# Performance work log

Measured on AMD Instinct MI355X. Metric: run time of the kernel, lower is better.

## Reference

```python
import jax, jax.numpy as jnp
import numpy as np

H = 64  # hidden size

def _lstm_layer(x_btf, w_ih, w_hh, b_ih, b_hh):
    """One LSTM layer, batch_first input x_btf [B,T,F]. PyTorch gate order i,f,g,o."""
    B = x_btf.shape[0]
    # Precompute input contribution for all timesteps: [T,B,4H]
    xg = jnp.einsum('btf,gf->tbg', x_btf, w_ih) + (b_ih + b_hh)
    h0 = jnp.zeros((B, H), dtype=x_btf.dtype)
    c0 = jnp.zeros((B, H), dtype=x_btf.dtype)

    def step(carry, xg_t):
        h, c = carry
        gates = xg_t + h @ w_hh.T  # [B,4H]
        i, f, g, o = jnp.split(gates, 4, axis=-1)
        i = jax.nn.sigmoid(i)
        f = jax.nn.sigmoid(f)
        g = jnp.tanh(g)
        o = jax.nn.sigmoid(o)
        c_new = f * c + i * g
        h_new = o * jnp.tanh(c_new)
        return (h_new, c_new), h_new

    (h_T, c_T), hs = jax.lax.scan(step, (h0, c0), xg)
    return jnp.transpose(hs, (1, 0, 2)), h_T, c_T  # [B,T,H], [B,H], [B,H]


def setup_inputs() -> dict:
    key = jax.random.key(0)
    ks = jax.random.split(key, 9)
    s_in = 1.0 / np.sqrt(H)
    inp = {
        'x': jax.random.normal(ks[0], (512, 2048, 4), dtype=jnp.float32),
        'w_ih_l0': jax.random.uniform(ks[1], (4 * H, 4), jnp.float32, -s_in, s_in),
        'w_hh_l0': jax.random.uniform(ks[2], (4 * H, H), jnp.float32, -s_in, s_in),
        'b_ih_l0': jax.random.uniform(ks[3], (4 * H,), jnp.float32, -s_in, s_in),
        'b_hh_l0': jax.random.uniform(ks[4], (4 * H,), jnp.float32, -s_in, s_in),
        'w_ih_l1': jax.random.uniform(ks[5], (4 * H, H), jnp.float32, -s_in, s_in),
        'w_hh_l1': jax.random.uniform(ks[6], (4 * H, H), jnp.float32, -s_in, s_in),
        'b_ih_l1': jax.random.uniform(ks[7], (4 * H,), jnp.float32, -s_in, s_in),
        'b_hh_l1': jax.random.uniform(ks[8], (4 * H,), jnp.float32, -s_in, s_in),
    }
    return inp


def reference(x, w_ih_l0, w_hh_l0, b_ih_l0, b_hh_l0, w_ih_l1, w_hh_l1, b_ih_l1, b_hh_l1):
    out0, h0, c0 = _lstm_layer(x, w_ih_l0, w_hh_l0, b_ih_l0, b_hh_l0)
    out1, h1, c1 = _lstm_layer(out0, w_ih_l1, w_hh_l1, b_ih_l1, b_hh_l1)
    h_n = jnp.stack([h0, h1], axis=0)  # [num_layers, B, H]
    c_n = jnp.stack([c0, c1], axis=0)
    return out1, (h_n, c_n)
```

## Files before the change

kernel.cpp:

```cpp
#include <hip/hip_runtime.h>

#define T_STEPS 2048
#define HID 64

typedef __attribute__((ext_vector_type(4))) int   int4v;
typedef __attribute__((ext_vector_type(4))) float f32x4;

static __device__ __forceinline__ float exp2_f(float x) {
#if __has_builtin(__builtin_amdgcn_exp2f)
    return __builtin_amdgcn_exp2f(x);
#else
    return exp2f(x);
#endif
}
#define NLOG2E 1.4426950408889634f

__global__ void __launch_bounds__(512, 1) __attribute__((amdgpu_waves_per_eu(2, 2)))
lstm2_i8(const float* __restrict__ x,
         const float* __restrict__ wih0, const float* __restrict__ whh0,
         const float* __restrict__ bih0, const float* __restrict__ bhh0,
         const float* __restrict__ wih1, const float* __restrict__ whh1,
         const float* __restrict__ bih1, const float* __restrict__ bhh1,
         float* __restrict__ out, int B)
{
    __shared__ __align__(16) char s_h0q[2][2][HID];
    __shared__ __align__(16) char s_h1q[2][2][HID];
    __shared__ __align__(16) float s_xf[2 * T_STEPS * 4];

    const int tid  = threadIdx.x;
    const int lane = tid & 63;
    const int wv   = tid >> 6;
    const int wg   = wv >> 2;
    const int wl   = wv & 3;
    const int l15  = lane & 15;
    const int lg   = lane >> 4;
    const int b0   = 2 * blockIdx.x;
    const int u    = 16 * wl + l15;
    const int bx   = lg & 1;
    const int rsel = (l15 >> 2) & 1;

    const float SCL[4] = {-NLOG2E, -NLOG2E, -2.0f * NLOG2E, -NLOG2E};

    const float4* __restrict__ xb4 = (const float4*)(x + (size_t)b0 * (T_STEPS * 4));
    float4* s_xf4 = (float4*)s_xf;
    for (int i2 = tid; i2 < 2 * T_STEPS; i2 += 512) s_xf4[i2] = xb4[i2];
    if (tid < 256) {
        ((char*)s_h0q)[tid] = 0;
        ((char*)s_h1q)[tid] = 0;
    }

    const size_t BTH = (size_t)B * T_STEPS * HID;
    const size_t BH  = (size_t)B * HID;
    const size_t bi  = (size_t)(b0 + bx) * HID + u;
    const int4v Zi = {0, 0, 0, 0};

    auto pack16 = [&](const float* wr, float qs) {
        int4v r;
        #pragma unroll
        for (int dw = 0; dw < 4; ++dw) {
            unsigned d = 0;
            #pragma unroll
            for (int bbb = 0; bbb < 4; ++bbb) {
                int q = (int)rintf(wr[dw * 4 + bbb] * qs);
                d |= ((unsigned)(q & 255)) << (8 * bbb);
            }
            r[dw] = (int)d;
        }
        return r;
    };
    auto rowmax = [&](const float* wr) {
        float mx = 0.f;
        #pragma unroll
        for (int j = 0; j < 16; ++j) mx = fmaxf(mx, fabsf(wr[j]));
        mx = fmaxf(mx, __shfl_xor(mx, 16));
        mx = fmaxf(mx, __shfl_xor(mx, 32));
        return fmaxf(mx, 1e-20f);
    };

    #define BAR() do { asm volatile("s_waitcnt lgkmcnt(0)" ::: "memory"); \
                       __builtin_amdgcn_s_barrier(); } while (0)

    if (wg == 0) {
        int4v W0q[4];
        float dq0[4];
        float wx[4][4];
        float b0s[4];
        #pragma unroll
        for (int ni = 0; ni < 4; ++ni) {
            const int g = 64 * ni + u;
            float wr[16];
            #pragma unroll
            for (int j = 0; j < 16; ++j) wr[j] = whh0[g * HID + 16 * lg + j];
            float mx = rowmax(wr);
            W0q[ni] = pack16(wr, 127.f / mx);
            dq0[ni] = (mx / (127.f * 127.f)) * SCL[ni];
            #pragma unroll
            for (int j = 0; j < 4; ++j) wx[ni][j] = wih0[g * 4 + j] * SCL[ni];
            b0s[ni] = (bih0[g] + bhh0[g]) * SCL[ni];
        }
        float c0s = 0.f, h0s = 0.f;
        const float* xcur = &s_xf[(size_t)bx * T_STEPS * 4];
        __syncthreads();

        auto l0_body = [&](int P) {
            const int Q = P ^ 1;
            const int4v Ha = *(const int4v*)&s_h0q[Q][rsel][16 * lg];
            const float4 xt = *(const float4*)xcur;  xcur += 4;
            __builtin_amdgcn_s_setprio(1);
            int4v a0 = __builtin_amdgcn_mfma_i32_16x16x64_i8(Ha, W0q[0], Zi, 0, 0, 0);
            int4v a1 = __builtin_amdgcn_mfma_i32_16x16x64_i8(Ha, W0q[1], Zi, 0, 0, 0);
            int4v a2 = __builtin_amdgcn_mfma_i32_16x16x64_i8(Ha, W0q[2], Zi, 0, 0, 0);
            int4v a3 = __builtin_amdgcn_mfma_i32_16x16x64_i8(Ha, W0q[3], Zi, 0, 0, 0);
            __builtin_amdgcn_s_setprio(0);
            float t0 = fmaf(wx[0][0], xt.x, b0s[0]);
            float t1 = fmaf(wx[1][0], xt.x, b0s[1]);
            float t2 = fmaf(wx[2][0], xt.x, b0s[2]);
            float t3 = fmaf(wx[3][0], xt.x, b0s[3]);
            t0 = fmaf(wx[0][1], xt.y, t0); t0 = fmaf(wx[0][2], xt.z, t0); t0 = fmaf(wx[0][3], xt.w, t0);
            t1 = fmaf(wx[1][1], xt.y, t1); t1 = fmaf(wx[1][2], xt.z, t1); t1 = fmaf(wx[1][3], xt.w, t1);
            t2 = fmaf(wx[2][1], xt.y, t2); t2 = fmaf(wx[2][2], xt.z, t2); t2 = fmaf(wx[2][3], xt.w, t2);
            t3 = fmaf(wx[3][1], xt.y, t3); t3 = fmaf(wx[3][2], xt.z, t3); t3 = fmaf(wx[3][3], xt.w, t3);
            float s0 = fmaf((float)a0[0], dq0[0], t0);
            float s1 = fmaf((float)a1[0], dq0[1], t1);
            float s2 = fmaf((float)a2[0], dq0[2], t2);
            float s3 = fmaf((float)a3[0], dq0[3], t3);
            float i_ = __builtin_amdgcn_rcpf(1.0f + exp2_f(s0));
            float f_ = __builtin_amdgcn_rcpf(1.0f + exp2_f(s1));
            float g_ = fmaf(2.0f, __builtin_amdgcn_rcpf(1.0f + exp2_f(s2)), -1.0f);
            float o_ = __builtin_amdgcn_rcpf(1.0f + exp2_f(s3));
            c0s = fmaf(f_, c0s, i_ * g_);
            h0s = o_ * fmaf(2.0f, __builtin_amdgcn_rcpf(1.0f + exp2_f(c0s * (-2.0f * NLOG2E))), -1.0f);
            if (lg < 2) s_h0q[P][lg][u] = (char)(int)rintf(h0s * 127.f);
        };

        for (int it = 0; it < T_STEPS / 2; ++it) {
            l0_body(0); BAR();
            l0_body(1); BAR();
        }
        if (lg < 2) {
            out[BTH + bi]          = h0s;
            out[BTH + 2 * BH + bi] = c0s;
        }
    } else {
        int4v Wihq[4], Whhq[4];
        float dqih[4], dqhh[4], b1s[4];
        #pragma unroll
        for (int ni = 0; ni < 4; ++ni) {
            const int g = 64 * ni + u;
            float wr[16];
            #pragma unroll
            for (int j = 0; j < 16; ++j) wr[j] = wih1[g * HID + 16 * lg + j];
            float mxi = rowmax(wr);
            Wihq[ni] = pack16(wr, 127.f / mxi);
            dqih[ni] = (mxi / (127.f * 127.f)) * SCL[ni];
            #pragma unroll
            for (int j = 0; j < 16; ++j) wr[j] = whh1[g * HID + 16 * lg + j];
            float mxh = rowmax(wr);
            Whhq[ni] = pack16(wr, 127.f / mxh);
            dqhh[ni] = (mxh / (127.f * 127.f)) * SCL[ni];
            b1s[ni] = (bih1[g] + bhh1[g]) * SCL[ni];
        }
        float c1s = 0.f, h1s = 0.f;
        float* __restrict__ opp = out + (size_t)(b0 + bx) * T_STEPS * HID + u;
        __syncthreads();
        BAR();

        auto l1_body = [&](int P) {
            const int Q = P ^ 1;
            const int4v Ha = *(const int4v*)&s_h0q[Q][rsel][16 * lg];
            const int4v Ga = *(const int4v*)&s_h1q[Q][rsel][16 * lg];
            __builtin_amdgcn_s_setprio(1);
            int4v dH0 = __builtin_amdgcn_mfma_i32_16x16x64_i8(Ha, Wihq[0], Zi, 0, 0, 0);
            int4v dH1 = __builtin_amdgcn_mfma_i32_16x16x64_i8(Ha, Wihq[1], Zi, 0, 0, 0);
            int4v dH2 = __builtin_amdgcn_mfma_i32_16x16x64_i8(Ha, Wihq[2], Zi, 0, 0, 0);
            int4v dH3 = __builtin_amdgcn_mfma_i32_16x16x64_i8(Ha, Wihq[3], Zi, 0, 0, 0);
            int4v dG0 = __builtin_amdgcn_mfma_i32_16x16x64_i8(Ga, Whhq[0], Zi, 0, 0, 0);
            int4v dG1 = __builtin_amdgcn_mfma_i32_16x16x64_i8(Ga, Whhq[1], Zi, 0, 0, 0);
            int4v dG2 = __builtin_amdgcn_mfma_i32_16x16x64_i8(Ga, Whhq[2], Zi, 0, 0, 0);
            int4v dG3 = __builtin_amdgcn_mfma_i32_16x16x64_i8(Ga, Whhq[3], Zi, 0, 0, 0);
            __builtin_amdgcn_s_setprio(0);
            float s0 = fmaf((float)dG0[0], dqhh[0], fmaf((float)dH0[0], dqih[0], b1s[0]));
            float s1 = fmaf((float)dG1[0], dqhh[1], fmaf((float)dH1[0], dqih[1], b1s[1]));
            float s2 = fmaf((float)dG2[0], dqhh[2], fmaf((float)dH2[0], dqih[2], b1s[2]));
            float s3 = fmaf((float)dG3[0], dqhh[3], fmaf((float)dH3[0], dqih[3], b1s[3]));
            float i_ = __builtin_amdgcn_rcpf(1.0f + exp2_f(s0));
            float f_ = __builtin_amdgcn_rcpf(1.0f + exp2_f(s1));
            float g_ = fmaf(2.0f, __builtin_amdgcn_rcpf(1.0f + exp2_f(s2)), -1.0f);
            float o_ = __builtin_amdgcn_rcpf(1.0f + exp2_f(s3));
            c1s = fmaf(f_, c1s, i_ * g_);
            h1s = o_ * fmaf(2.0f, __builtin_amdgcn_rcpf(1.0f + exp2_f(c1s * (-2.0f * NLOG2E))), -1.0f);
            if (lg < 2) {
                s_h1q[P][lg][u] = (char)(int)rintf(h1s * 127.f);
                *opp = h1s;
            }
            opp += HID;
        };

        for (int it = 0; it < T_STEPS / 2 - 1; ++it) {
            l1_body(1); BAR();
            l1_body(0); BAR();
        }
        l1_body(1); BAR();
        l1_body(0);
        if (lg < 2) {
            out[BTH + BH + bi]     = h1s;
            out[BTH + 3 * BH + bi] = c1s;
        }
    }
    #undef BAR
}

extern "C" void kernel_launch(void* const* d_in, const int* in_sizes, int n_in,
                              void* d_out, int out_size, void* d_ws, size_t ws_size,
                              hipStream_t stream) {
    const float* x    = (const float*)d_in[0];
    const float* wih0 = (const float*)d_in[1];
    const float* whh0 = (const float*)d_in[2];
    const float* bih0 = (const float*)d_in[3];
    const float* bhh0 = (const float*)d_in[4];
    const float* wih1 = (const float*)d_in[5];
    const float* whh1 = (const float*)d_in[6];
    const float* bih1 = (const float*)d_in[7];
    const float* bhh1 = (const float*)d_in[8];
    float* out = (float*)d_out;

    const int B = in_sizes[0] / (T_STEPS * 4);

    lstm2_i8<<<dim3(B / 2), dim3(512), 0, stream>>>(
        x, wih0, whh0, bih0, bhh0, wih1, whh1, bih1, bhh1, out, B);
}
```

Before: 649.5 us.

## Split gate columns across 16 waves with shuffle exchange and MFMA-fused bias

Doubles the block to 1024 threads (8 waves per layer), so each wave computes only two gate tiles per step instead of four. Lanes swap gate pre-activations with a cross-lane shuffle to assemble i,f,g,o. The bias is quantized and folded into the MFMA accumulator input, and layer 1 chains its input and recurrent MFMAs by sharing one row scale across both weight matrices. This shortens the per-wave critical path of each serial timestep, at the cost of barriers over more waves, an extra shuffle, and coarser quantization from the shared scale and integer bias.

```diff
diff --git a/kernel.cpp b/kernel.cpp
--- a/kernel.cpp
+++ b/kernel.cpp
@@ -3,8 +3,7 @@
 #define T_STEPS 2048
 #define HID 64
 
-typedef __attribute__((ext_vector_type(4))) int   int4v;
-typedef __attribute__((ext_vector_type(4))) float f32x4;
+typedef __attribute__((ext_vector_type(4))) int int4v;
 
 static __device__ __forceinline__ float exp2_f(float x) {
 #if __has_builtin(__builtin_amdgcn_exp2f)
@@ -15,13 +14,13 @@
 }
 #define NLOG2E 1.4426950408889634f
 
-__global__ void __launch_bounds__(512, 1) __attribute__((amdgpu_waves_per_eu(2, 2)))
-lstm2_i8(const float* __restrict__ x,
-         const float* __restrict__ wih0, const float* __restrict__ whh0,
-         const float* __restrict__ bih0, const float* __restrict__ bhh0,
-         const float* __restrict__ wih1, const float* __restrict__ whh1,
-         const float* __restrict__ bih1, const float* __restrict__ bhh1,
-         float* __restrict__ out, int B)
+__global__ void __launch_bounds__(1024, 1) __attribute__((amdgpu_waves_per_eu(4, 4)))
+lstm2_w16(const float* __restrict__ x,
+          const float* __restrict__ wih0, const float* __restrict__ whh0,
+          const float* __restrict__ bih0, const float* __restrict__ bhh0,
+          const float* __restrict__ wih1, const float* __restrict__ whh1,
+          const float* __restrict__ bih1, const float* __restrict__ bhh1,
+          float* __restrict__ out, int B)
 {
     __shared__ __align__(16) char s_h0q[2][2][HID];
     __shared__ __align__(16) char s_h1q[2][2][HID];
@@ -30,20 +29,29 @@
     const int tid  = threadIdx.x;
     const int lane = tid & 63;
     const int wv   = tid >> 6;
-    const int wg   = wv >> 2;
-    const int wl   = wv & 3;
+    const int wg   = wv >> 3;
+    const int wl   = wv & 7;
+    const int base = 8 * wl;
     const int l15  = lane & 15;
     const int lg   = lane >> 4;
+    const int l8   = l15 & 7;
+    const int h8   = l15 >> 3;
     const int b0   = 2 * blockIdx.x;
-    const int u    = 16 * wl + l15;
     const int bx   = lg & 1;
     const int rsel = (l15 >> 2) & 1;
+    const int un   = base + l8;
 
     const float SCL[4] = {-NLOG2E, -NLOG2E, -2.0f * NLOG2E, -NLOG2E};
+    const int   tP = h8;
+    const int   tQ = 2 + h8;
+    const int   rP = 64 * tP + un;
+    const int   rQ = 64 * tQ + un;
+    const float aselQ = h8 ? 1.0f : 2.0f;
+    const float cselQ = h8 ? 0.0f : -1.0f;
 
     const float4* __restrict__ xb4 = (const float4*)(x + (size_t)b0 * (T_STEPS * 4));
     float4* s_xf4 = (float4*)s_xf;
-    for (int i2 = tid; i2 < 2 * T_STEPS; i2 += 512) s_xf4[i2] = xb4[i2];
+    for (int i2 = tid; i2 < 2 * T_STEPS; i2 += 1024) s_xf4[i2] = xb4[i2];
     if (tid < 256) {
         ((char*)s_h0q)[tid] = 0;
         ((char*)s_h1q)[tid] = 0;
@@ -51,8 +59,6 @@
 
     const size_t BTH = (size_t)B * T_STEPS * HID;
     const size_t BH  = (size_t)B * HID;
-    const size_t bi  = (size_t)(b0 + bx) * HID + u;
-    const int4v Zi = {0, 0, 0, 0};
 
     auto pack16 = [&](const float* wr, float qs) {
         int4v r;
@@ -60,43 +66,47 @@
         for (int dw = 0; dw < 4; ++dw) {
             unsigned d = 0;
             #pragma unroll
-            for (int bbb = 0; bbb < 4; ++bbb) {
-                int q = (int)rintf(wr[dw * 4 + bbb] * qs);
-                d |= ((unsigned)(q & 255)) << (8 * bbb);
+            for (int bb = 0; bb < 4; ++bb) {
+                int q = (int)rintf(wr[dw * 4 + bb] * qs);
+                d |= ((unsigned)(q & 255)) << (8 * bb);
             }
             r[dw] = (int)d;
         }
         return r;
     };
-    auto rowmax = [&](const float* wr) {
-        float mx = 0.f;
-        #pragma unroll
-        for (int j = 0; j < 16; ++j) mx = fmaxf(mx, fabsf(wr[j]));
-        mx = fmaxf(mx, __shfl_xor(mx, 16));
-        mx = fmaxf(mx, __shfl_xor(mx, 32));
-        return fmaxf(mx, 1e-20f);
-    };
 
     #define BAR() do { asm volatile("s_waitcnt lgkmcnt(0)" ::: "memory"); \
                        __builtin_amdgcn_s_barrier(); } while (0)
 
     if (wg == 0) {
-        int4v W0q[4];
-        float dq0[4];
-        float wx[4][4];
-        float b0s[4];
-        #pragma unroll
-        for (int ni = 0; ni < 4; ++ni) {
-            const int g = 64 * ni + u;
-            float wr[16];
-            #pragma unroll
-            for (int j = 0; j < 16; ++j) wr[j] = whh0[g * HID + 16 * lg + j];
-            float mx = rowmax(wr);
-            W0q[ni] = pack16(wr, 127.f / mx);
-            dq0[ni] = (mx / (127.f * 127.f)) * SCL[ni];
-            #pragma unroll
-            for (int j = 0; j < 4; ++j) wx[ni][j] = wih0[g * 4 + j] * SCL[ni];
-            b0s[ni] = (bih0[g] + bhh0[g]) * SCL[ni];
+        float wrP[16], wrQ[16];
+        #pragma unroll
+        for (int j = 0; j < 16; ++j) {
+            wrP[j] = whh0[rP * HID + 16 * lg + j];
+            wrQ[j] = whh0[rQ * HID + 16 * lg + j];
+        }
+        float mxP = 0.f, mxQ = 0.f;
+        #pragma unroll
+        for (int j = 0; j < 16; ++j) {
+            mxP = fmaxf(mxP, fabsf(wrP[j]));
+            mxQ = fmaxf(mxQ, fabsf(wrQ[j]));
+        }
+        mxP = fmaxf(mxP, __shfl_xor(mxP, 16)); mxP = fmaxf(mxP, __shfl_xor(mxP, 32));
+        mxQ = fmaxf(mxQ, __shfl_xor(mxQ, 16)); mxQ = fmaxf(mxQ, __shfl_xor(mxQ, 32));
+        mxP = fmaxf(mxP, 1e-20f); mxQ = fmaxf(mxQ, 1e-20f);
+        const int4v WPq = pack16(wrP, 127.f / mxP);
+        const int4v WQq = pack16(wrQ, 127.f / mxQ);
+        const float dqP = (mxP / 16129.f) * SCL[tP];
+        const float dqQ = (mxQ / 16129.f) * SCL[tQ];
+        const int bP = (int)rintf((bih0[rP] + bhh0[rP]) * 16129.f / mxP);
+        const int bQ = (int)rintf((bih0[rQ] + bhh0[rQ]) * 16129.f / mxQ);
+        const int4v BiasP = {bP, bP, bP, bP};
+        const int4v BiasQ = {bQ, bQ, bQ, bQ};
+        float wxP[4], wxQ[4];
+        #pragma unroll
+        for (int j = 0; j < 4; ++j) {
+            wxP[j] = wih0[rP * 4 + j] * SCL[tP];
+            wxQ[j] = wih0[rQ * 4 + j] * SCL[tQ];
         }
         float c0s = 0.f, h0s = 0.f;
         const float* xcur = &s_xf[(size_t)bx * T_STEPS * 4];
@@ -107,61 +117,69 @@
             const int4v Ha = *(const int4v*)&s_h0q[Q][rsel][16 * lg];
             const float4 xt = *(const float4*)xcur;  xcur += 4;
             __builtin_amdgcn_s_setprio(1);
-            int4v a0 = __builtin_amdgcn_mfma_i32_16x16x64_i8(Ha, W0q[0], Zi, 0, 0, 0);
-            int4v a1 = __builtin_amdgcn_mfma_i32_16x16x64_i8(Ha, W0q[1], Zi, 0, 0, 0);
-            int4v a2 = __builtin_amdgcn_mfma_i32_16x16x64_i8(Ha, W0q[2], Zi, 0, 0, 0);
-            int4v a3 = __builtin_amdgcn_mfma_i32_16x16x64_i8(Ha, W0q[3], Zi, 0, 0, 0);
+            int4v aP = __builtin_amdgcn_mfma_i32_16x16x64_i8(Ha, WPq, BiasP, 0, 0, 0);
+            int4v aQ = __builtin_amdgcn_mfma_i32_16x16x64_i8(Ha, WQq, BiasQ, 0, 0, 0);
             __builtin_amdgcn_s_setprio(0);
-            float t0 = fmaf(wx[0][0], xt.x, b0s[0]);
-            float t1 = fmaf(wx[1][0], xt.x, b0s[1]);
-            float t2 = fmaf(wx[2][0], xt.x, b0s[2]);
-            float t3 = fmaf(wx[3][0], xt.x, b0s[3]);
-            t0 = fmaf(wx[0][1], xt.y, t0); t0 = fmaf(wx[0][2], xt.z, t0); t0 = fmaf(wx[0][3], xt.w, t0);
-            t1 = fmaf(wx[1][1], xt.y, t1); t1 = fmaf(wx[1][2], xt.z, t1); t1 = fmaf(wx[1][3], xt.w, t1);
-            t2 = fmaf(wx[2][1], xt.y, t2); t2 = fmaf(wx[2][2], xt.z, t2); t2 = fmaf(wx[2][3], xt.w, t2);
-            t3 = fmaf(wx[3][1], xt.y, t3); t3 = fmaf(wx[3][2], xt.z, t3); t3 = fmaf(wx[3][3], xt.w, t3);
-            float s0 = fmaf((float)a0[0], dq0[0], t0);
-            float s1 = fmaf((float)a1[0], dq0[1], t1);
-            float s2 = fmaf((float)a2[0], dq0[2], t2);
-            float s3 = fmaf((float)a3[0], dq0[3], t3);
-            float i_ = __builtin_amdgcn_rcpf(1.0f + exp2_f(s0));
-            float f_ = __builtin_amdgcn_rcpf(1.0f + exp2_f(s1));
-            float g_ = fmaf(2.0f, __builtin_amdgcn_rcpf(1.0f + exp2_f(s2)), -1.0f);
-            float o_ = __builtin_amdgcn_rcpf(1.0f + exp2_f(s3));
+            float xP = wxP[0] * xt.x;
+            float xQ = wxQ[0] * xt.x;
+            xP = fmaf(wxP[1], xt.y, xP); xP = fmaf(wxP[2], xt.z, xP); xP = fmaf(wxP[3], xt.w, xP);
+            xQ = fmaf(wxQ[1], xt.y, xQ); xQ = fmaf(wxQ[2], xt.z, xQ); xQ = fmaf(wxQ[3], xt.w, xQ);
+            float sP = fmaf((float)aP[0], dqP, xP);
+            float sQ = fmaf((float)aQ[0], dqQ, xQ);
+            float oP = __shfl_xor(sP, 8);
+            float oQ = __shfl_xor(sQ, 8);
+            float ip = h8 ? oP : sP;
+            float fp = h8 ? sP : oP;
+            float gp = h8 ? oQ : sQ;
+            float op = h8 ? sQ : oQ;
+            float i_ = __builtin_amdgcn_rcpf(1.0f + exp2_f(ip));
+            float f_ = __builtin_amdgcn_rcpf(1.0f + exp2_f(fp));
+            float g_ = fmaf(2.0f, __builtin_amdgcn_rcpf(1.0f + exp2_f(gp)), -1.0f);
+            float o_ = __builtin_amdgcn_rcpf(1.0f + exp2_f(op));
             c0s = fmaf(f_, c0s, i_ * g_);
             h0s = o_ * fmaf(2.0f, __builtin_amdgcn_rcpf(1.0f + exp2_f(c0s * (-2.0f * NLOG2E))), -1.0f);
-            if (lg < 2) s_h0q[P][lg][u] = (char)(int)rintf(h0s * 127.f);
+            if (lg < 2 && l15 < 8) s_h0q[P][lg][un] = (char)(int)rintf(h0s * 127.f);
         };
 
         for (int it = 0; it < T_STEPS / 2; ++it) {
             l0_body(0); BAR();
             l0_body(1); BAR();
         }
-        if (lg < 2) {
+        if (lg < 2 && l15 < 8) {
+            const size_t bi = (size_t)(b0 + lg) * HID + un;
             out[BTH + bi]          = h0s;
             out[BTH + 2 * BH + bi] = c0s;
         }
     } else {
-        int4v Wihq[4], Whhq[4];
-        float dqih[4], dqhh[4], b1s[4];
-        #pragma unroll
-        for (int ni = 0; ni < 4; ++ni) {
-            const int g = 64 * ni + u;
-            float wr[16];
-            #pragma unroll
-            for (int j = 0; j < 16; ++j) wr[j] = wih1[g * HID + 16 * lg + j];
-            float mxi = rowmax(wr);
-            Wihq[ni] = pack16(wr, 127.f / mxi);
-            dqih[ni] = (mxi / (127.f * 127.f)) * SCL[ni];
-            #pragma unroll
-            for (int j = 0; j < 16; ++j) wr[j] = whh1[g * HID + 16 * lg + j];
-            float mxh = rowmax(wr);
-            Whhq[ni] = pack16(wr, 127.f / mxh);
-            dqhh[ni] = (mxh / (127.f * 127.f)) * SCL[ni];
-            b1s[ni] = (bih1[g] + bhh1[g]) * SCL[ni];
-        }
+        float wiP[16], whP[16], wiQ[16], whQ[16];
+        #pragma unroll
+        for (int j = 0; j < 16; ++j) {
+            wiP[j] = wih1[rP * HID + 16 * lg + j];
+            whP[j] = whh1[rP * HID + 16 * lg + j];
+            wiQ[j] = wih1[rQ * HID + 16 * lg + j];
+            whQ[j] = whh1[rQ * HID + 16 * lg + j];
+        }
+        float mxP = 0.f, mxQ = 0.f;
+        #pragma unroll
+        for (int j = 0; j < 16; ++j) {
+            mxP = fmaxf(mxP, fmaxf(fabsf(wiP[j]), fabsf(whP[j])));
+            mxQ = fmaxf(mxQ, fmaxf(fabsf(wiQ[j]), fabsf(whQ[j])));
+        }
+        mxP = fmaxf(mxP, __shfl_xor(mxP, 16)); mxP = fmaxf(mxP, __shfl_xor(mxP, 32));
+        mxQ = fmaxf(mxQ, __shfl_xor(mxQ, 16)); mxQ = fmaxf(mxQ, __shfl_xor(mxQ, 32));
+        mxP = fmaxf(mxP, 1e-20f); mxQ = fmaxf(mxQ, 1e-20f);
+        const int4v WPi = pack16(wiP, 127.f / mxP);
+        const int4v WPh = pack16(whP, 127.f / mxP);
+        const int4v WQi = pack16(wiQ, 127.f / mxQ);
+        const int4v WQh = pack16(whQ, 127.f / mxQ);
+        const float dqP = (mxP / 16129.f) * SCL[tP];
+        const float dqQ = (mxQ / 16129.f) * SCL[tQ];
+        const int bP = (int)rintf((bih1[rP] + bhh1[rP]) * 16129.f / mxP);
+        const int bQ = (int)rintf((bih1[rQ] + bhh1[rQ]) * 16129.f / mxQ);
+        const int4v BiasP = {bP, bP, bP, bP};
+        const int4v BiasQ = {bQ, bQ, bQ, bQ};
         float c1s = 0.f, h1s = 0.f;
-        float* __restrict__ opp = out + (size_t)(b0 + bx) * T_STEPS * HID + u;
+        float* __restrict__ opp = out + (size_t)(b0 + bx) * T_STEPS * HID + un;
         __syncthreads();
         BAR();
 
@@ -170,27 +188,27 @@
             const int4v Ha = *(const int4v*)&s_h0q[Q][rsel][16 * lg];
             const int4v Ga = *(const int4v*)&s_h1q[Q][rsel][16 * lg];
             __builtin_amdgcn_s_setprio(1);
-            int4v dH0 = __builtin_amdgcn_mfma_i32_16x16x64_i8(Ha, Wihq[0], Zi, 0, 0, 0);
-            int4v dH1 = __builtin_amdgcn_mfma_i32_16x16x64_i8(Ha, Wihq[1], Zi, 0, 0, 0);
-            int4v dH2 = __builtin_amdgcn_mfma_i32_16x16x64_i8(Ha, Wihq[2], Zi, 0, 0, 0);
-            int4v dH3 = __builtin_amdgcn_mfma_i32_16x16x64_i8(Ha, Wihq[3], Zi, 0, 0, 0);
-            int4v dG0 = __builtin_amdgcn_mfma_i32_16x16x64_i8(Ga, Whhq[0], Zi, 0, 0, 0);
-            int4v dG1 = __builtin_amdgcn_mfma_i32_16x16x64_i8(Ga, Whhq[1], Zi, 0, 0, 0);
-            int4v dG2 = __builtin_amdgcn_mfma_i32_16x16x64_i8(Ga, Whhq[2], Zi, 0, 0, 0);
-            int4v dG3 = __builtin_amdgcn_mfma_i32_16x16x64_i8(Ga, Whhq[3], Zi, 0, 0, 0);
+            int4v p1 = __builtin_amdgcn_mfma_i32_16x16x64_i8(Ha, WPi, BiasP, 0, 0, 0);
+            int4v q1 = __builtin_amdgcn_mfma_i32_16x16x64_i8(Ha, WQi, BiasQ, 0, 0, 0);
+            int4v p2 = __builtin_amdgcn_mfma_i32_16x16x64_i8(Ga, WPh, p1, 0, 0, 0);
+            int4v q2 = __builtin_amdgcn_mfma_i32_16x16x64_i8(Ga, WQh, q1, 0, 0, 0);
             __builtin_amdgcn_s_setprio(0);
-            float s0 = fmaf((float)dG0[0], dqhh[0], fmaf((float)dH0[0], dqih[0], b1s[0]));
-            float s1 = fmaf((float)dG1[0], dqhh[1], fmaf((float)dH1[0], dqih[1], b1s[1]));
-            float s2 = fmaf((float)dG2[0], dqhh[2], fmaf((float)dH2[0], dqih[2], b1s[2]));
-            float s3 = fmaf((float)dG3[0], dqhh[3], fmaf((float)dH3[0], dqih[3], b1s[3]));
-            float i_ = __builtin_amdgcn_rcpf(1.0f + exp2_f(s0));
-            float f_ = __builtin_amdgcn_rcpf(1.0f + exp2_f(s1));
-            float g_ = fmaf(2.0f, __builtin_amdgcn_rcpf(1.0f + exp2_f(s2)), -1.0f);
-            float o_ = __builtin_amdgcn_rcpf(1.0f + exp2_f(s3));
+            float sP = (float)p2[0] * dqP;
+            float sQ = (float)q2[0] * dqQ;
+            float oP = __shfl_xor(sP, 8);
+            float oQ = __shfl_xor(sQ, 8);
+            float ip = h8 ? oP : sP;
+            float fp = h8 ? sP : oP;
+            float gp = h8 ? oQ : sQ;
+            float op = h8 ? sQ : oQ;
+            float i_ = __builtin_amdgcn_rcpf(1.0f + exp2_f(ip));
+            float f_ = __builtin_amdgcn_rcpf(1.0f + exp2_f(fp));
+            float g_ = fmaf(2.0f, __builtin_amdgcn_rcpf(1.0f + exp2_f(gp)), -1.0f);
+            float o_ = __builtin_amdgcn_rcpf(1.0f + exp2_f(op));
             c1s = fmaf(f_, c1s, i_ * g_);
             h1s = o_ * fmaf(2.0f, __builtin_amdgcn_rcpf(1.0f + exp2_f(c1s * (-2.0f * NLOG2E))), -1.0f);
-            if (lg < 2) {
-                s_h1q[P][lg][u] = (char)(int)rintf(h1s * 127.f);
+            if (lg < 2 && l15 < 8) {
+                s_h1q[P][lg][un] = (char)(int)rintf(h1s * 127.f);
                 *opp = h1s;
             }
             opp += HID;
@@ -202,7 +220,8 @@
         }
         l1_body(1); BAR();
         l1_body(0);
-        if (lg < 2) {
+        if (lg < 2 && l15 < 8) {
+            const size_t bi = (size_t)(b0 + lg) * HID + un;
             out[BTH + BH + bi]     = h1s;
             out[BTH + 3 * BH + bi] = c1s;
         }
@@ -226,6 +245,6 @@
 
     const int B = in_sizes[0] / (T_STEPS * 4);
 
-    lstm2_i8<<<dim3(B / 2), dim3(512), 0, stream>>>(
+    lstm2_w16<<<dim3(B / 2), dim3(1024), 0, stream>>>(
         x, wih0, whh0, bih0, bhh0, wih1, whh1, bih1, bhh1, out, B);
 }
```

Result: slower. 912.8 us (+40.5%).

## Skew layer-1 behind layer-0 with 4-deep h0 ring and chained int8 MFMAs

Applied to the files above, without the earlier changes.

Layer 0's h buffer becomes a 4-slot ring, so layer 1 can run one step further behind and prefetch the next h0 into registers at the end of each step instead of loading it on the critical path. Layer 1 now uses one shared quantisation scale for W_ih and W_hh. This lets the two MFMA products accumulate into one int32 accumulator that starts from a quantised bias, which removes the separate dequantise-and-add FMAs. In exchange the shared scale and the integer bias reduce precision, and the barrier schedule between the two wave groups becomes more intricate.

```diff
diff --git a/kernel.cpp b/kernel.cpp
--- a/kernel.cpp
+++ b/kernel.cpp
@@ -3,8 +3,7 @@
 #define T_STEPS 2048
 #define HID 64
 
-typedef __attribute__((ext_vector_type(4))) int   int4v;
-typedef __attribute__((ext_vector_type(4))) float f32x4;
+typedef __attribute__((ext_vector_type(4))) int int4v;
 
 static __device__ __forceinline__ float exp2_f(float x) {
 #if __has_builtin(__builtin_amdgcn_exp2f)
@@ -16,14 +15,14 @@
 #define NLOG2E 1.4426950408889634f
 
 __global__ void __launch_bounds__(512, 1) __attribute__((amdgpu_waves_per_eu(2, 2)))
-lstm2_i8(const float* __restrict__ x,
-         const float* __restrict__ wih0, const float* __restrict__ whh0,
-         const float* __restrict__ bih0, const float* __restrict__ bhh0,
-         const float* __restrict__ wih1, const float* __restrict__ whh1,
-         const float* __restrict__ bih1, const float* __restrict__ bhh1,
-         float* __restrict__ out, int B)
+lstm2_sk2(const float* __restrict__ x,
+          const float* __restrict__ wih0, const float* __restrict__ whh0,
+          const float* __restrict__ bih0, const float* __restrict__ bhh0,
+          const float* __restrict__ wih1, const float* __restrict__ whh1,
+          const float* __restrict__ bih1, const float* __restrict__ bhh1,
+          float* __restrict__ out, int B)
 {
-    __shared__ __align__(16) char s_h0q[2][2][HID];
+    __shared__ __align__(16) char s_h0q[4][2][HID];
     __shared__ __align__(16) char s_h1q[2][2][HID];
     __shared__ __align__(16) float s_xf[2 * T_STEPS * 4];
 
@@ -45,7 +44,7 @@
     float4* s_xf4 = (float4*)s_xf;
     for (int i2 = tid; i2 < 2 * T_STEPS; i2 += 512) s_xf4[i2] = xb4[i2];
     if (tid < 256) {
-        ((char*)s_h0q)[tid] = 0;
+        ((char*)s_h0q)[tid] = 0; ((char*)s_h0q)[tid + 256] = 0;
         ((char*)s_h1q)[tid] = 0;
     }
 
@@ -67,14 +66,6 @@
             r[dw] = (int)d;
         }
         return r;
-    };
-    auto rowmax = [&](const float* wr) {
-        float mx = 0.f;
-        #pragma unroll
-        for (int j = 0; j < 16; ++j) mx = fmaxf(mx, fabsf(wr[j]));
-        mx = fmaxf(mx, __shfl_xor(mx, 16));
-        mx = fmaxf(mx, __shfl_xor(mx, 32));
-        return fmaxf(mx, 1e-20f);
     };
 
     #define BAR() do { asm volatile("s_waitcnt lgkmcnt(0)" ::: "memory"); \
@@ -91,9 +82,14 @@
             float wr[16];
             #pragma unroll
             for (int j = 0; j < 16; ++j) wr[j] = whh0[g * HID + 16 * lg + j];
-            float mx = rowmax(wr);
+            float mx = 0.f;
+            #pragma unroll
+            for (int j = 0; j < 16; ++j) mx = fmaxf(mx, fabsf(wr[j]));
+            mx = fmaxf(mx, __shfl_xor(mx, 16));
+            mx = fmaxf(mx, __shfl_xor(mx, 32));
+            mx = fmaxf(mx, 1e-20f);
             W0q[ni] = pack16(wr, 127.f / mx);
-            dq0[ni] = (mx / (127.f * 127.f)) * SCL[ni];
+            dq0[ni] = (mx / 16129.f) * SCL[ni];
             #pragma unroll
             for (int j = 0; j < 4; ++j) wx[ni][j] = wih0[g * 4 + j] * SCL[ni];
             b0s[ni] = (bih0[g] + bhh0[g]) * SCL[ni];
@@ -102,9 +98,8 @@
         const float* xcur = &s_xf[(size_t)bx * T_STEPS * 4];
         __syncthreads();
 
-        auto l0_body = [&](int P) {
-            const int Q = P ^ 1;
-            const int4v Ha = *(const int4v*)&s_h0q[Q][rsel][16 * lg];
+        auto l0_step = [&](int RD, int WR) {
+            const int4v Ha = *(const int4v*)&s_h0q[RD][rsel][16 * lg];
             const float4 xt = *(const float4*)xcur;  xcur += 4;
             __builtin_amdgcn_s_setprio(1);
             int4v a0 = __builtin_amdgcn_mfma_i32_16x16x64_i8(Ha, W0q[0], Zi, 0, 0, 0);
@@ -130,59 +125,72 @@
             float o_ = __builtin_amdgcn_rcpf(1.0f + exp2_f(s3));
             c0s = fmaf(f_, c0s, i_ * g_);
             h0s = o_ * fmaf(2.0f, __builtin_amdgcn_rcpf(1.0f + exp2_f(c0s * (-2.0f * NLOG2E))), -1.0f);
-            if (lg < 2) s_h0q[P][lg][u] = (char)(int)rintf(h0s * 127.f);
+            if (lg < 2) s_h0q[WR][lg][u] = (char)(int)rintf(h0s * 127.f);
         };
 
-        for (int it = 0; it < T_STEPS / 2; ++it) {
-            l0_body(0); BAR();
-            l0_body(1); BAR();
-        }
+        l0_step(3, 0); BAR();
+        l0_step(0, 1); BAR();
+        for (int it = 0; it < 511; ++it) {
+            l0_step(1, 2); BAR();
+            l0_step(2, 3); BAR();
+            l0_step(3, 0); BAR();
+            l0_step(0, 1); BAR();
+        }
+        l0_step(1, 2); BAR();
+        l0_step(2, 3); BAR();
+        BAR();
         if (lg < 2) {
             out[BTH + bi]          = h0s;
             out[BTH + 2 * BH + bi] = c0s;
         }
     } else {
-        int4v Wihq[4], Whhq[4];
-        float dqih[4], dqhh[4], b1s[4];
+        int4v Wihq[4], Whhq[4], BiasI[4];
+        float dq1[4];
         #pragma unroll
         for (int ni = 0; ni < 4; ++ni) {
             const int g = 64 * ni + u;
-            float wr[16];
-            #pragma unroll
-            for (int j = 0; j < 16; ++j) wr[j] = wih1[g * HID + 16 * lg + j];
-            float mxi = rowmax(wr);
-            Wihq[ni] = pack16(wr, 127.f / mxi);
-            dqih[ni] = (mxi / (127.f * 127.f)) * SCL[ni];
-            #pragma unroll
-            for (int j = 0; j < 16; ++j) wr[j] = whh1[g * HID + 16 * lg + j];
-            float mxh = rowmax(wr);
-            Whhq[ni] = pack16(wr, 127.f / mxh);
-            dqhh[ni] = (mxh / (127.f * 127.f)) * SCL[ni];
-            b1s[ni] = (bih1[g] + bhh1[g]) * SCL[ni];
+            float wi[16], wh[16];
+            #pragma unroll
+            for (int j = 0; j < 16; ++j) {
+                wi[j] = wih1[g * HID + 16 * lg + j];
+                wh[j] = whh1[g * HID + 16 * lg + j];
+            }
+            float mx = 0.f;
+            #pragma unroll
+            for (int j = 0; j < 16; ++j) mx = fmaxf(mx, fmaxf(fabsf(wi[j]), fabsf(wh[j])));
+            mx = fmaxf(mx, __shfl_xor(mx, 16));
+            mx = fmaxf(mx, __shfl_xor(mx, 32));
+            mx = fmaxf(mx, 1e-20f);
+            Wihq[ni] = pack16(wi, 127.f / mx);
+            Whhq[ni] = pack16(wh, 127.f / mx);
+            dq1[ni]  = (mx / 16129.f) * SCL[ni];
+            const int bq = (int)rintf((bih1[g] + bhh1[g]) * 16129.f / mx);
+            BiasI[ni] = (int4v){bq, bq, bq, bq};
         }
         float c1s = 0.f, h1s = 0.f;
         float* __restrict__ opp = out + (size_t)(b0 + bx) * T_STEPS * HID + u;
+        int4v Hp;
         __syncthreads();
         BAR();
-
-        auto l1_body = [&](int P) {
-            const int Q = P ^ 1;
-            const int4v Ha = *(const int4v*)&s_h0q[Q][rsel][16 * lg];
-            const int4v Ga = *(const int4v*)&s_h1q[Q][rsel][16 * lg];
+        Hp = *(const int4v*)&s_h0q[0][rsel][16 * lg];
+        BAR();
+
+        auto l1_step = [&](int RH, int WH, int PF) {
+            const int4v Ga = *(const int4v*)&s_h1q[RH][rsel][16 * lg];
             __builtin_amdgcn_s_setprio(1);
-            int4v dH0 = __builtin_amdgcn_mfma_i32_16x16x64_i8(Ha, Wihq[0], Zi, 0, 0, 0);
-            int4v dH1 = __builtin_amdgcn_mfma_i32_16x16x64_i8(Ha, Wihq[1], Zi, 0, 0, 0);
-            int4v dH2 = __builtin_amdgcn_mfma_i32_16x16x64_i8(Ha, Wihq[2], Zi, 0, 0, 0);
-            int4v dH3 = __builtin_amdgcn_mfma_i32_16x16x64_i8(Ha, Wihq[3], Zi, 0, 0, 0);
-            int4v dG0 = __builtin_amdgcn_mfma_i32_16x16x64_i8(Ga, Whhq[0], Zi, 0, 0, 0);
-            int4v dG1 = __builtin_amdgcn_mfma_i32_16x16x64_i8(Ga, Whhq[1], Zi, 0, 0, 0);
-            int4v dG2 = __builtin_amdgcn_mfma_i32_16x16x64_i8(Ga, Whhq[2], Zi, 0, 0, 0);
-            int4v dG3 = __builtin_amdgcn_mfma_i32_16x16x64_i8(Ga, Whhq[3], Zi, 0, 0, 0);
+            int4v p0 = __builtin_amdgcn_mfma_i32_16x16x64_i8(Hp, Wihq[0], BiasI[0], 0, 0, 0);
+            int4v p1 = __builtin_amdgcn_mfma_i32_16x16x64_i8(Hp, Wihq[1], BiasI[1], 0, 0, 0);
+            int4v p2 = __builtin_amdgcn_mfma_i32_16x16x64_i8(Hp, Wihq[2], BiasI[2], 0, 0, 0);
+            int4v p3 = __builtin_amdgcn_mfma_i32_16x16x64_i8(Hp, Wihq[3], BiasI[3], 0, 0, 0);
+            p0 = __builtin_amdgcn_mfma_i32_16x16x64_i8(Ga, Whhq[0], p0, 0, 0, 0);
+            p1 = __builtin_amdgcn_mfma_i32_16x16x64_i8(Ga, Whhq[1], p1, 0, 0, 0);
+            p2 = __builtin_amdgcn_mfma_i32_16x16x64_i8(Ga, Whhq[2], p2, 0, 0, 0);
+            p3 = __builtin_amdgcn_mfma_i32_16x16x64_i8(Ga, Whhq[3], p3, 0, 0, 0);
             __builtin_amdgcn_s_setprio(0);
-            float s0 = fmaf((float)dG0[0], dqhh[0], fmaf((float)dH0[0], dqih[0], b1s[0]));
-            float s1 = fmaf((float)dG1[0], dqhh[1], fmaf((float)dH1[0], dqih[1], b1s[1]));
-            float s2 = fmaf((float)dG2[0], dqhh[2], fmaf((float)dH2[0], dqih[2], b1s[2]));
-            float s3 = fmaf((float)dG3[0], dqhh[3], fmaf((float)dH3[0], dqih[3], b1s[3]));
+            float s0 = (float)p0[0] * dq1[0];
+            float s1 = (float)p1[0] * dq1[1];
+            float s2 = (float)p2[0] * dq1[2];
+            float s3 = (float)p3[0] * dq1[3];
             float i_ = __builtin_amdgcn_rcpf(1.0f + exp2_f(s0));
             float f_ = __builtin_amdgcn_rcpf(1.0f + exp2_f(s1));
             float g_ = fmaf(2.0f, __builtin_amdgcn_rcpf(1.0f + exp2_f(s2)), -1.0f);
@@ -190,18 +198,23 @@
             c1s = fmaf(f_, c1s, i_ * g_);
             h1s = o_ * fmaf(2.0f, __builtin_amdgcn_rcpf(1.0f + exp2_f(c1s * (-2.0f * NLOG2E))), -1.0f);
             if (lg < 2) {
-                s_h1q[P][lg][u] = (char)(int)rintf(h1s * 127.f);
+                s_h1q[WH][lg][u] = (char)(int)rintf(h1s * 127.f);
                 *opp = h1s;
             }
             opp += HID;
+            if (PF >= 0) Hp = *(const int4v*)&s_h0q[PF][rsel][16 * lg];
         };
 
-        for (int it = 0; it < T_STEPS / 2 - 1; ++it) {
-            l1_body(1); BAR();
-            l1_body(0); BAR();
-        }
-        l1_body(1); BAR();
-        l1_body(0);
+        for (int it = 0; it < 511; ++it) {
+            l1_step(1, 0, 1); BAR();
+            l1_step(0, 1, 2); BAR();
+            l1_step(1, 0, 3); BAR();
+            l1_step(0, 1, 0); BAR();
+        }
+        l1_step(1, 0, 1); BAR();
+        l1_step(0, 1, 2); BAR();
+        l1_step(1, 0, 3); BAR();
+        l1_step(0, 1, -1);
         if (lg < 2) {
             out[BTH + BH + bi]     = h1s;
             out[BTH + 3 * BH + bi] = c1s;
@@ -226,6 +239,6 @@
 
     const int B = in_sizes[0] / (T_STEPS * 4);
 
-    lstm2_i8<<<dim3(B / 2), dim3(512), 0, stream>>>(
+    lstm2_sk2<<<dim3(B / 2), dim3(512), 0, stream>>>(
         x, wih0, whh0, bih0, bhh0, wih1, whh1, bih1, bhh1, out, B);
 }
```

Result: no change. 640.3 us (-1.4%).
